# Kernel optimization log

Hardware: AMD Instinct MI355X
Metric: run time of the kernel (lower is better)

Reference implementation:

```python
import jax, jax.numpy as jnp
import numpy as np

B, T, V = 2, 2048, 256
C, H, L = 1024, 16, 8
DH = C // H  # 64


def setup_inputs() -> dict:
    key = jax.random.key(0)
    ks = jax.random.split(key, 12)
    s = 0.02
    return {
        "x": jax.random.normal(ks[0], (B, T, V), jnp.float32),
        "W_emb": jax.random.normal(ks[1], (V, C), jnp.float32) * s,
        "b_emb": jnp.zeros((C,), jnp.float32),
        "pos": jax.random.normal(ks[2], (1, T, C), jnp.float32) * s,
        "Wqkv": jax.random.normal(ks[3], (L, C, 3 * C), jnp.float32) * s,
        "bqkv": jnp.zeros((L, 3 * C), jnp.float32),
        "Wproj": jax.random.normal(ks[4], (L, C, C), jnp.float32) * s,
        "bproj": jnp.zeros((L, C), jnp.float32),
        "gamma": jnp.ones((C,), jnp.float32),
        "beta": jnp.zeros((C,), jnp.float32),
        "W_out": jax.random.normal(ks[5], (C, V), jnp.float32) * s,
        "b_out": jnp.zeros((V,), jnp.float32),
    }


def _attn_block(h, Wqkv_l, bqkv_l, Wproj_l, bproj_l):
    # h: [B, T, C]
    qkv = h @ Wqkv_l + bqkv_l                      # [B, T, 3C]
    q, k, v = jnp.split(qkv, 3, axis=-1)
    q = q.reshape(B, T, H, DH)
    k = k.reshape(B, T, H, DH)
    v = v.reshape(B, T, H, DH)
    scale = 1.0 / np.sqrt(DH).astype(np.float32)
    att = jnp.einsum("bthd,bshd->bhts", q, k) * scale   # [B, H, T, T]
    att = jax.nn.softmax(att, axis=-1)
    y = jnp.einsum("bhts,bshd->bthd", att, v)            # [B, T, H, DH]
    y = y.reshape(B, T, C)
    return y @ Wproj_l + bproj_l


def reference(x, W_emb, b_emb, pos, Wqkv, bqkv, Wproj, bproj, gamma, beta, W_out, b_out):
    h = x @ W_emb + b_emb            # dense embedding: Linear(V -> C)
    h = h + pos[:, :T, :]
    # NOTE: original blocks return attention output directly (no residual, no MLP)
    def body(h, params):
        Wq, bq, Wp, bp = params
        return _attn_block(h, Wq, bq, Wp, bp), None
    h, _ = jax.lax.scan(body, h, (Wqkv, bqkv, Wproj, bproj))
    # LayerNorm
    mu = jnp.mean(h, axis=-1, keepdims=True)
    var = jnp.mean(jnp.square(h - mu), axis=-1, keepdims=True)
    h = (h - mu) * jax.lax.rsqrt(var + 1e-5) * gamma + beta
    return h @ W_out + b_out          # [B, T, V]
```

## Files before the change

### kernel.cpp

```cpp
#include <hip/hip_runtime.h>
#include <hip/hip_bf16.h>

#define T_SEQ 2048
#define BATCH 2
#define CDIM 1024
#define VDIM 256
#define NHEAD 16
#define DHEAD 64
#define NLAYER 8
#define MROWS (BATCH * T_SEQ)

typedef __attribute__((ext_vector_type(8))) short bf16x8;
typedef __attribute__((ext_vector_type(4))) float f32x4;
typedef __attribute__((ext_vector_type(4))) int i32x4;

#define SELHI 0x07060302u
#define SELLO 0x05040100u
#define QSCALE 0.18033688011112042f

__device__ __forceinline__ uint prm(uint a, uint b, uint s) { return __builtin_amdgcn_perm(a, b, s); }

__device__ __forceinline__ uint bf16rne(float f) {
    uint u = __float_as_uint(f);
    return (u + 0x7fffu + ((u >> 16) & 1u)) & 0xffff0000u;
}
__device__ __forceinline__ uint packsplit(float x) {
    uint hb = bf16rne(x);
    float d = x - __uint_as_float(hb);
    uint lb = bf16rne(d);
    return prm(hb, lb, SELHI);
}
__device__ __forceinline__ float unpack2(uint u) {
    return __uint_as_float(u & 0xffff0000u) + __uint_as_float(u << 16);
}
__device__ __forceinline__ bf16x8 asb(i32x4 v) {
    union { i32x4 i; bf16x8 b; } u; u.i = v; return u.b;
}
__device__ __forceinline__ short bfs(float f) { return (short)(bf16rne(f) >> 16); }


__global__ __launch_bounds__(256) void packx_kernel(
    const float* __restrict__ x, uint* __restrict__ xpf)
{
    const int t  = blockIdx.x * 256 + threadIdx.x;
    const int m  = t >> 6;
    const int k0 = (t & 63) * 4;
    const float4 v = *(const float4*)&x[(size_t)m * 256 + k0];
    const size_t addr = ((size_t)(m >> 4) * 8 + (k0 >> 5)) * 512
                      + (size_t)(((k0 >> 2) & 3) * 16 + (m & 15)) * 8
                      + 4 * ((k0 >> 4) & 1);
    uint4 pk;
    pk.x = packsplit(v.x); pk.y = packsplit(v.y);
    pk.z = packsplit(v.z); pk.w = packsplit(v.w);
    *(uint4*)&xpf[addr] = pk;
}

__global__ __launch_bounds__(256) void wsplit_kernel(
    const float* __restrict__ W, short* __restrict__ Fh, short* __restrict__ Fl,
    int N, int K)
{
    const int ln = threadIdx.x & 63, lk = threadIdx.x >> 6;
    const int n  = blockIdx.x * 64 + ln;
    const int kq = blockIdx.y * 4 + lk;
    const int k0 = kq * 4;

    float f0 = W[(size_t)(k0 + 0) * N + n];
    float f1 = W[(size_t)(k0 + 1) * N + n];
    float f2 = W[(size_t)(k0 + 2) * N + n];
    float f3 = W[(size_t)(k0 + 3) * N + n];
    uint h0 = bf16rne(f0), h1 = bf16rne(f1), h2 = bf16rne(f2), h3 = bf16rne(f3);

    const int gl = kq & 3, j0 = ((kq >> 2) & 1) * 4;
    const size_t base = (((size_t)(n >> 4) * (K >> 5) + (kq >> 3)) * 64 + gl * 16 + (n & 15)) * 8 + j0;
    *(int2*)&Fh[base] = make_int2((int)prm(h1, h0, SELHI), (int)prm(h3, h2, SELHI));
    if (Fl) {
        uint l0 = bf16rne(f0 - __uint_as_float(h0));
        uint l1 = bf16rne(f1 - __uint_as_float(h1));
        uint l2 = bf16rne(f2 - __uint_as_float(h2));
        uint l3 = bf16rne(f3 - __uint_as_float(h3));
        *(int2*)&Fl[base] = make_int2((int)prm(l1, l0, SELHI), (int)prm(l3, l2, SELHI));
    }
}

template <int TERMS>
__global__ __launch_bounds__(256) void gemm_mfma_kernel(
    const uint* __restrict__ Apf, const short* __restrict__ Ahf,
    const short* __restrict__ Bhf, const short* __restrict__ Blf,
    const float* __restrict__ bias, const float* __restrict__ addrow,
    uint* __restrict__ Cv, short* __restrict__ Chf,
    uint* __restrict__ Cq, short* __restrict__ Ckf,
    short* __restrict__ Cvf, int M, int N, int K, int out_mode)
{
    const int tid = threadIdx.x, lane = tid & 63, w = tid >> 6;
    const int wr = w >> 1, wc = w & 1, x = lane & 15, gl = lane >> 4;
    const int bm = blockIdx.y * 128, bn = blockIdx.x * 128;
    const int nkc = K >> 5;

    const uint*  ab  = Apf ? Apf + ((size_t)((bm >> 4) + wr * 4) * nkc) * 512 + (size_t)lane * 8 : nullptr;
    const short* abh = Ahf ? Ahf + (((size_t)((bm >> 4) + wr * 4) * nkc) * 64 + lane) * 8 : nullptr;
    const short* hb  = Bhf + (((size_t)((bn >> 4) + wc * 4) * nkc) * 64 + lane) * 8;
    const short* lb  = Blf + (((size_t)((bn >> 4) + wc * 4) * nkc) * 64 + lane) * 8;
    const size_t tstrA = (size_t)nkc * 512;
    const size_t tstrF = (size_t)nkc * 512;

    f32x4 acc[4][4];
#pragma unroll
    for (int mi = 0; mi < 4; ++mi)
#pragma unroll
        for (int ni = 0; ni < 4; ++ni) acc[mi][ni] = (f32x4){0.f, 0.f, 0.f, 0.f};

    for (int kc = 0; kc < nkc; ++kc) {
        const size_t ko = (size_t)kc * 512;
        bf16x8 ah[4], al[4], bh[4], bl[4];
#pragma unroll
        for (int t = 0; t < 4; ++t) {
            if (TERMS == 1) {
                ah[t] = *(const bf16x8*)(abh + t * tstrF + ko);
            } else {
                const uint* ap = ab + t * tstrA + ko;
                uint4 a0 = *(const uint4*)ap;
                uint4 a1 = *(const uint4*)(ap + 4);
                i32x4 h4, l4;
                h4[0] = (int)prm(a0.y, a0.x, SELHI); h4[1] = (int)prm(a0.w, a0.z, SELHI);
                h4[2] = (int)prm(a1.y, a1.x, SELHI); h4[3] = (int)prm(a1.w, a1.z, SELHI);
                l4[0] = (int)prm(a0.y, a0.x, SELLO); l4[1] = (int)prm(a0.w, a0.z, SELLO);
                l4[2] = (int)prm(a1.y, a1.x, SELLO); l4[3] = (int)prm(a1.w, a1.z, SELLO);
                ah[t] = asb(h4); al[t] = asb(l4);
            }
            bh[t] = *(const bf16x8*)(hb + t * tstrF + ko);
            if (TERMS >= 3) bl[t] = *(const bf16x8*)(lb + t * tstrF + ko);
        }
        __builtin_amdgcn_s_setprio(1);
#pragma unroll
        for (int mi = 0; mi < 4; ++mi)
#pragma unroll
            for (int ni = 0; ni < 4; ++ni) {
                acc[mi][ni] = __builtin_amdgcn_mfma_f32_16x16x32_bf16(ah[mi], bh[ni], acc[mi][ni], 0, 0, 0);
                if (TERMS >= 3)
                    acc[mi][ni] = __builtin_amdgcn_mfma_f32_16x16x32_bf16(ah[mi], bl[ni], acc[mi][ni], 0, 0, 0);
                if (TERMS >= 2)
                    acc[mi][ni] = __builtin_amdgcn_mfma_f32_16x16x32_bf16(al[mi], bh[ni], acc[mi][ni], 0, 0, 0);
            }
        __builtin_amdgcn_s_setprio(0);
    }

#pragma unroll
    for (int ni = 0; ni < 4; ++ni) {
        const int n = bn + wc * 64 + ni * 16 + x;
        const float bv = bias[n];
#pragma unroll
        for (int mi = 0; mi < 4; ++mi) {
            const int m0 = bm + wr * 64 + mi * 16 + gl * 4;
            const f32x4 o = acc[mi][ni];
            if (out_mode == 0) {
                float* C = (float*)Cv;
                C[(size_t)(m0 + 0) * N + n] = o[0] + bv;
                C[(size_t)(m0 + 1) * N + n] = o[1] + bv;
                C[(size_t)(m0 + 2) * N + n] = o[2] + bv;
                C[(size_t)(m0 + 3) * N + n] = o[3] + bv;
            } else if (out_mode == 2) {
                float p0 = 0.f, p1 = 0.f, p2 = 0.f, p3 = 0.f;
                if (addrow) {
                    p0 = addrow[(size_t)((m0 + 0) & (T_SEQ - 1)) * N + n];
                    p1 = addrow[(size_t)((m0 + 1) & (T_SEQ - 1)) * N + n];
                    p2 = addrow[(size_t)((m0 + 2) & (T_SEQ - 1)) * N + n];
                    p3 = addrow[(size_t)((m0 + 3) & (T_SEQ - 1)) * N + n];
                }
                const float v0 = o[0] + bv + p0, v1 = o[1] + bv + p1;
                const float v2 = o[2] + bv + p2, v3 = o[3] + bv + p3;
                const size_t mt = (size_t)(bm >> 4) + wr * 4 + mi;
                const size_t base = (mt * (N >> 5) + (n >> 5)) * 512
                                  + (size_t)(((n >> 2) & 3) * 16 + gl * 4) * 8
                                  + (n & 3) + 4 * ((n >> 4) & 1);
                Cv[base + 0 * 8] = packsplit(v0);
                Cv[base + 1 * 8] = packsplit(v1);
                Cv[base + 2 * 8] = packsplit(v2);
                Cv[base + 3 * 8] = packsplit(v3);
                if (Chf) {
                    const size_t fb = ((mt * (N >> 5) + (n >> 5)) * 64
                                      + ((n >> 2) & 3) * 16 + gl * 4) * 8
                                      + (n & 3) + 4 * ((n >> 4) & 1);
                    Chf[fb + 0 * 8] = bfs(v0);
                    Chf[fb + 1 * 8] = bfs(v1);
                    Chf[fb + 2 * 8] = bfs(v2);
                    Chf[fb + 3 * 8] = bfs(v3);
                }
            } else if (n < 1024) {
                Cq[(size_t)(m0 + 0) * 1024 + n] = packsplit((o[0] + bv) * QSCALE);
                Cq[(size_t)(m0 + 1) * 1024 + n] = packsplit((o[1] + bv) * QSCALE);
                Cq[(size_t)(m0 + 2) * 1024 + n] = packsplit((o[2] + bv) * QSCALE);
                Cq[(size_t)(m0 + 3) * 1024 + n] = packsplit((o[3] + bv) * QSCALE);
            } else if (n < 2048) {
                const int dd6 = n - 1024;
                const int hhh = dd6 >> 6, ch = (dd6 >> 5) & 1, dd = dd6 & 31;
                const int bq = m0 >> 11, sv = m0 & (T_SEQ - 1);
                const size_t base = ((((size_t)(bq * NHEAD + hhh) * 128 + (sv >> 4)) * 2 + ch) * 64
                                    + 16 * ((dd & 15) >> 2) + (sv & 15)) * 8
                                    + (dd & 3) + 4 * (dd >> 4);
                Ckf[base + 0]  = bfs(o[0] + bv);
                Ckf[base + 8]  = bfs(o[1] + bv);
                Ckf[base + 16] = bfs(o[2] + bv);
                Ckf[base + 24] = bfs(o[3] + bv);
            } else {
                const int dd6 = n - 2048;
                const int hhh = dd6 >> 6, dmi = (dd6 >> 4) & 3, xt = dd6 & 15;
                const int bq = m0 >> 11, sv = m0 & (T_SEQ - 1);
                const size_t base = ((((size_t)(bq * NHEAD + hhh) * 64 + (sv >> 5)) * 4 + dmi) * 64
                                    + xt + 16 * ((sv & 15) >> 2)) * 8 + 4 * ((sv >> 4) & 1);
                short4 st;
                st.x = bfs(o[0] + bv); st.y = bfs(o[1] + bv);
                st.z = bfs(o[2] + bv); st.w = bfs(o[3] + bv);
                *(short4*)&Cvf[base] = st;
            }
        }
    }
}

__global__ __launch_bounds__(256) void attn_mfma_kernel(
    const uint* __restrict__ qrow, const short* __restrict__ kf,
    const short* __restrict__ vf, uint* __restrict__ y)
{
    const int tid  = threadIdx.x;
    const int w    = tid >> 6;
    const int lane = tid & 63;
    const int x    = lane & 15;
    const int gl   = lane >> 4;

    const int orig = blockIdx.x;
    const int wgid = (orig & 7) * 64 + (orig >> 3);
    const int bh = wgid >> 4;
    const int b = bh >> 4, hh = bh & 15;
    const int t0 = (wgid & 15) * 128;

    i32x4 qhi[2][2];
#pragma unroll
    for (int qf = 0; qf < 2; ++qf) {
        const uint* qp = qrow + (size_t)(b * T_SEQ + t0 + 64 * qf + 16 * w + x) * 1024 + hh * 64;
#pragma unroll
        for (int ch = 0; ch < 2; ++ch) {
            uint4 a0 = *(const uint4*)(qp + 32 * ch + 4 * gl);
            uint4 a1 = *(const uint4*)(qp + 32 * ch + 16 + 4 * gl);
            qhi[qf][ch][0] = (int)prm(a0.y, a0.x, SELHI); qhi[qf][ch][1] = (int)prm(a0.w, a0.z, SELHI);
            qhi[qf][ch][2] = (int)prm(a1.y, a1.x, SELHI); qhi[qf][ch][3] = (int)prm(a1.w, a1.z, SELHI);
        }
    }

    const short* kb = kf + (size_t)bh * 128 * 2 * 512 + (size_t)lane * 8;
    const short* vb = vf + (size_t)bh * 64 * 4 * 512 + (size_t)lane * 8;

    i32x4 ones4;
    ones4[0] = ones4[1] = ones4[2] = ones4[3] = 0x3F803F80;

    f32x4 oacc[2][4], lacc[2];
#pragma unroll
    for (int qf = 0; qf < 2; ++qf) {
        lacc[qf] = (f32x4){0.f, 0.f, 0.f, 0.f};
#pragma unroll
        for (int i = 0; i < 4; ++i) oacc[qf][i] = (f32x4){0.f, 0.f, 0.f, 0.f};
    }

    for (int s0 = 0; s0 < T_SEQ; s0 += 64) {
        bf16x8 kh[4][2], vh[2][4];
#pragma unroll
        for (int sc = 0; sc < 4; ++sc)
#pragma unroll
            for (int ch = 0; ch < 2; ++ch)
                kh[sc][ch] = *(const bf16x8*)(kb + ((((size_t)(s0 >> 4) + sc) * 2 + ch) * 512));
#pragma unroll
        for (int ch = 0; ch < 2; ++ch)
#pragma unroll
            for (int dm = 0; dm < 4; ++dm)
                vh[ch][dm] = *(const bf16x8*)(vb + ((((size_t)(s0 >> 5) + ch) * 4 + dm) * 512));

#pragma unroll
        for (int qf = 0; qf < 2; ++qf) {
            f32x4 s4[4];
#pragma unroll
            for (int sc = 0; sc < 4; ++sc) {
                s4[sc] = (f32x4){0.f, 0.f, 0.f, 0.f};
                s4[sc] = __builtin_amdgcn_mfma_f32_16x16x32_bf16(kh[sc][0], asb(qhi[qf][0]), s4[sc], 0, 0, 0);
                s4[sc] = __builtin_amdgcn_mfma_f32_16x16x32_bf16(kh[sc][1], asb(qhi[qf][1]), s4[sc], 0, 0, 0);
            }
#pragma unroll
            for (int sc = 0; sc < 4; ++sc) {
                s4[sc][0] = __builtin_amdgcn_exp2f(s4[sc][0]);
                s4[sc][1] = __builtin_amdgcn_exp2f(s4[sc][1]);
                s4[sc][2] = __builtin_amdgcn_exp2f(s4[sc][2]);
                s4[sc][3] = __builtin_amdgcn_exp2f(s4[sc][3]);
            }
            i32x4 pfh[2];
#pragma unroll
            for (int c = 0; c < 2; ++c) {
                f32x4 pa = s4[2 * c], pb = s4[2 * c + 1];
                pfh[c][0] = (int)prm(__float_as_uint(pa[1]), __float_as_uint(pa[0]), SELHI);
                pfh[c][1] = (int)prm(__float_as_uint(pa[3]), __float_as_uint(pa[2]), SELHI);
                pfh[c][2] = (int)prm(__float_as_uint(pb[1]), __float_as_uint(pb[0]), SELHI);
                pfh[c][3] = (int)prm(__float_as_uint(pb[3]), __float_as_uint(pb[2]), SELHI);
            }
            lacc[qf] = __builtin_amdgcn_mfma_f32_16x16x32_bf16(asb(ones4), asb(pfh[0]), lacc[qf], 0, 0, 0);
            lacc[qf] = __builtin_amdgcn_mfma_f32_16x16x32_bf16(asb(ones4), asb(pfh[1]), lacc[qf], 0, 0, 0);
#pragma unroll
            for (int dm = 0; dm < 4; ++dm) {
                oacc[qf][dm] = __builtin_amdgcn_mfma_f32_16x16x32_bf16(vh[0][dm], asb(pfh[0]), oacc[qf][dm], 0, 0, 0);
                oacc[qf][dm] = __builtin_amdgcn_mfma_f32_16x16x32_bf16(vh[1][dm], asb(pfh[1]), oacc[qf][dm], 0, 0, 0);
            }
        }
    }

#pragma unroll
    for (int qf = 0; qf < 2; ++qf) {
        const float invl = 1.f / lacc[qf][0];
        const size_t mt = (size_t)((b * T_SEQ + t0) >> 4) + 4 * qf + w;
#pragma unroll
        for (int dm = 0; dm < 4; ++dm) {
            f32x4 o = oacc[qf][dm];
            const size_t addr = (mt * 32 + hh * 2 + (dm >> 1)) * 512
                              + (size_t)lane * 8 + 4 * (dm & 1);
            uint4 pk;
            pk.x = packsplit(o[0] * invl); pk.y = packsplit(o[1] * invl);
            pk.z = packsplit(o[2] * invl); pk.w = packsplit(o[3] * invl);
            *(uint4*)&y[addr] = pk;
        }
    }
}

__global__ __launch_bounds__(256) void ln_kernel(
    const uint* __restrict__ h, const float* __restrict__ gamma,
    const float* __restrict__ beta, uint* __restrict__ outp)
{
    const int row = blockIdx.x;
    const int tid = threadIdx.x;

    const size_t addr = ((size_t)(row >> 4) * 32 + (tid >> 3)) * 512
                      + (size_t)((tid & 3) * 16 + (row & 15)) * 8
                      + 4 * ((tid >> 2) & 1);
    uint4 u = *(const uint4*)&h[addr];
    float4 v;
    v.x = unpack2(u.x); v.y = unpack2(u.y); v.z = unpack2(u.z); v.w = unpack2(u.w);

    float s  = v.x + v.y + v.z + v.w;
    float ss = v.x * v.x + v.y * v.y + v.z * v.z + v.w * v.w;
#pragma unroll
    for (int off = 1; off < 64; off <<= 1) {
        s  += __shfl_xor(s, off);
        ss += __shfl_xor(ss, off);
    }
    __shared__ float rs[4], rss[4];
    const int wid = tid >> 6;
    if ((tid & 63) == 0) { rs[wid] = s; rss[wid] = ss; }
    __syncthreads();
    s  = rs[0] + rs[1] + rs[2] + rs[3];
    ss = rss[0] + rss[1] + rss[2] + rss[3];

    const float mu   = s * (1.f / (float)CDIM);
    const float var  = ss * (1.f / (float)CDIM) - mu * mu;
    const float rstd = rsqrtf(var + 1e-5f);

    const float4 g  = *(const float4*)&gamma[tid * 4];
    const float4 be = *(const float4*)&beta[tid * 4];
    uint4 pk;
    pk.x = packsplit((v.x - mu) * rstd * g.x + be.x);
    pk.y = packsplit((v.y - mu) * rstd * g.y + be.y);
    pk.z = packsplit((v.z - mu) * rstd * g.z + be.z);
    pk.w = packsplit((v.w - mu) * rstd * g.w + be.w);
    *(uint4*)&outp[addr] = pk;
}

extern "C" void kernel_launch(void* const* d_in, const int* in_sizes, int n_in,
                              void* d_out, int out_size, void* d_ws, size_t ws_size,
                              hipStream_t stream)
{
    const float* x      = (const float*)d_in[0];
    const float* W_emb  = (const float*)d_in[1];
    const float* b_emb  = (const float*)d_in[2];
    const float* pos    = (const float*)d_in[3];
    const float* Wqkv   = (const float*)d_in[4];
    const float* bqkv   = (const float*)d_in[5];
    const float* Wproj  = (const float*)d_in[6];
    const float* bproj  = (const float*)d_in[7];
    const float* gamma  = (const float*)d_in[8];
    const float* beta   = (const float*)d_in[9];
    const float* W_out  = (const float*)d_in[10];
    const float* b_out  = (const float*)d_in[11];
    float* out = (float*)d_out;

    uint* h    = (uint*)d_ws;
    uint* qrow = h + (size_t)MROWS * CDIM;
    uint* y    = qrow + (size_t)MROWS * CDIM;
    short* kf  = (short*)(y + (size_t)MROWS * CDIM);
    short* vfb = kf + (size_t)32 * 128 * 2 * 512;
    short* hf  = vfb + (size_t)32 * 64 * 4 * 512;
    short* Bqh = hf + (size_t)MROWS * CDIM;
    short* Bph = Bqh + (size_t)3 * CDIM * CDIM;
    short* Bpl = Bph + (size_t)CDIM * CDIM;
    short* Eh  = Bpl + (size_t)CDIM * CDIM;
    short* El  = Eh  + (size_t)VDIM * CDIM;
    short* Oh  = El  + (size_t)VDIM * CDIM;
    short* Ol  = Oh  + (size_t)CDIM * VDIM;
    uint*  xpf = (uint*)(Ol + (size_t)CDIM * VDIM);

    const dim3 blk(256);
    const int nattn = (T_SEQ / 128) * BATCH * NHEAD;

    packx_kernel<<<dim3(MROWS * (VDIM / 4) / 256), blk, 0, stream>>>(x, xpf);
    wsplit_kernel<<<dim3(CDIM / 64, VDIM / 16), blk, 0, stream>>>(W_emb, Eh, El, CDIM, VDIM);
    gemm_mfma_kernel<3><<<dim3(CDIM / 128, MROWS / 128), blk, 0, stream>>>(
        xpf, nullptr, Eh, El, b_emb, pos, h, hf, nullptr, nullptr, nullptr, MROWS, CDIM, VDIM, 2);

    for (int l = 0; l < NLAYER; ++l) {
        wsplit_kernel<<<dim3(3 * CDIM / 64, CDIM / 16), blk, 0, stream>>>(
            Wqkv + (size_t)l * CDIM * 3 * CDIM, Bqh, nullptr, 3 * CDIM, CDIM);
        gemm_mfma_kernel<1><<<dim3(3 * CDIM / 128, MROWS / 128), blk, 0, stream>>>(
            nullptr, hf, Bqh, nullptr, bqkv + (size_t)l * 3 * CDIM, nullptr,
            nullptr, nullptr, qrow, kf, vfb, MROWS, 3 * CDIM, CDIM, 3);
        attn_mfma_kernel<<<dim3(nattn), blk, 0, stream>>>(qrow, kf, vfb, y);
        wsplit_kernel<<<dim3(CDIM / 64, CDIM / 16), blk, 0, stream>>>(
            Wproj + (size_t)l * CDIM * CDIM, Bph, Bpl, CDIM, CDIM);
        gemm_mfma_kernel<3><<<dim3(CDIM / 128, MROWS / 128), blk, 0, stream>>>(
            y, nullptr, Bph, Bpl, bproj + (size_t)l * CDIM, nullptr,
            h, hf, nullptr, nullptr, nullptr, MROWS, CDIM, CDIM, 2);
    }

    ln_kernel<<<dim3(MROWS), blk, 0, stream>>>(h, gamma, beta, y);
    wsplit_kernel<<<dim3(VDIM / 64, CDIM / 16), blk, 0, stream>>>(W_out, Oh, Ol, VDIM, CDIM);
    gemm_mfma_kernel<3><<<dim3(VDIM / 128, MROWS / 128), blk, 0, stream>>>(
        y, nullptr, Oh, Ol, b_out, nullptr, (uint*)out, nullptr, nullptr, nullptr, nullptr, MROWS, VDIM, CDIM, 0);
}
```

Before: 1.092 ms.

## Stage QKV GEMM operands through LDS via direct global-to-LDS loads

Adds a dedicated single-term QKV projection GEMM in which each k-step copies the A and B fragment tiles into shared memory with global_load_lds, then has the four waves read them from LDS. Previously every wave loaded its own fragments straight from global memory, so each tile was fetched twice per block. Sharing through LDS halves global/L2 traffic per block, at the cost of two barriers per k-step and no double buffering, which may leave load latency exposed. The generic GEMM loses its QKV output mode.

Result: no change. 1.086 ms (-0.6%).

```diff
diff --git a/kernel.cpp b/kernel.cpp
--- a/kernel.cpp
+++ b/kernel.cpp
@@ -37,6 +37,11 @@
     union { i32x4 i; bf16x8 b; } u; u.i = v; return u.b;
 }
 __device__ __forceinline__ short bfs(float f) { return (short)(bf16rne(f) >> 16); }
+__device__ __forceinline__ void gload_lds16(const void* g, void* l) {
+    __builtin_amdgcn_global_load_lds(
+        (const __attribute__((address_space(1))) void*)g,
+        (__attribute__((address_space(3))) void*)l, 16, 0, 0);
+}
 
 
 __global__ __launch_bounds__(256) void packx_kernel(
@@ -82,14 +87,100 @@
     }
 }
 
+__global__ __launch_bounds__(256) void gemm_lds1_kernel(
+    const short* __restrict__ Ahf, const short* __restrict__ Bhf,
+    const float* __restrict__ bias,
+    uint* __restrict__ Cq, short* __restrict__ Ckf, short* __restrict__ Cvf,
+    int M, int N, int K)
+{
+    __shared__ __align__(16) short Asm[8][64][8];
+    __shared__ __align__(16) short Bsm[8][64][8];
+
+    const int tid = threadIdx.x, lane = tid & 63, w = tid >> 6;
+    const int wr = w >> 1, wc = w & 1, x = lane & 15, gl = lane >> 4;
+    const int bm = blockIdx.y * 128, bn = blockIdx.x * 128;
+    const int nkc = K >> 5;
+    const size_t tstr = (size_t)nkc * 512;
+
+    const short* sbase = (w < 2)
+        ? Ahf + ((size_t)((bm >> 4) + 4 * w) * nkc) * 512 + (size_t)lane * 8
+        : Bhf + ((size_t)((bn >> 4) + 4 * (w - 2)) * nkc) * 512 + (size_t)lane * 8;
+    short* dbase = (w < 2) ? &Asm[4 * w][0][0] : &Bsm[4 * (w - 2)][0][0];
+
+    f32x4 acc[4][4];
+#pragma unroll
+    for (int mi = 0; mi < 4; ++mi)
+#pragma unroll
+        for (int ni = 0; ni < 4; ++ni) acc[mi][ni] = (f32x4){0.f, 0.f, 0.f, 0.f};
+
+    for (int kc = 0; kc < nkc; ++kc) {
+        __syncthreads();
+#pragma unroll
+        for (int i = 0; i < 4; ++i)
+            gload_lds16(sbase + i * tstr + (size_t)kc * 512, dbase + i * 512);
+        __syncthreads();
+
+        bf16x8 ah[4], bh[4];
+#pragma unroll
+        for (int t = 0; t < 4; ++t) {
+            ah[t] = *(const bf16x8*)&Asm[wr * 4 + t][lane][0];
+            bh[t] = *(const bf16x8*)&Bsm[wc * 4 + t][lane][0];
+        }
+        __builtin_amdgcn_s_setprio(1);
+#pragma unroll
+        for (int mi = 0; mi < 4; ++mi)
+#pragma unroll
+            for (int ni = 0; ni < 4; ++ni)
+                acc[mi][ni] = __builtin_amdgcn_mfma_f32_16x16x32_bf16(ah[mi], bh[ni], acc[mi][ni], 0, 0, 0);
+        __builtin_amdgcn_s_setprio(0);
+    }
+
+#pragma unroll
+    for (int ni = 0; ni < 4; ++ni) {
+        const int n = bn + wc * 64 + ni * 16 + x;
+        const float bv = bias[n];
+#pragma unroll
+        for (int mi = 0; mi < 4; ++mi) {
+            const int m0 = bm + wr * 64 + mi * 16 + gl * 4;
+            const f32x4 o = acc[mi][ni];
+            if (n < 1024) {
+                Cq[(size_t)(m0 + 0) * 1024 + n] = packsplit((o[0] + bv) * QSCALE);
+                Cq[(size_t)(m0 + 1) * 1024 + n] = packsplit((o[1] + bv) * QSCALE);
+                Cq[(size_t)(m0 + 2) * 1024 + n] = packsplit((o[2] + bv) * QSCALE);
+                Cq[(size_t)(m0 + 3) * 1024 + n] = packsplit((o[3] + bv) * QSCALE);
+            } else if (n < 2048) {
+                const int dd6 = n - 1024;
+                const int hhh = dd6 >> 6, ch = (dd6 >> 5) & 1, dd = dd6 & 31;
+                const int bq = m0 >> 11, sv = m0 & (T_SEQ - 1);
+                const size_t base = ((((size_t)(bq * NHEAD + hhh) * 128 + (sv >> 4)) * 2 + ch) * 64
+                                    + 16 * ((dd & 15) >> 2) + (sv & 15)) * 8
+                                    + (dd & 3) + 4 * (dd >> 4);
+                Ckf[base + 0]  = bfs(o[0] + bv);
+                Ckf[base + 8]  = bfs(o[1] + bv);
+                Ckf[base + 16] = bfs(o[2] + bv);
+                Ckf[base + 24] = bfs(o[3] + bv);
+            } else {
+                const int dd6 = n - 2048;
+                const int hhh = dd6 >> 6, dmi = (dd6 >> 4) & 3, xt = dd6 & 15;
+                const int bq = m0 >> 11, sv = m0 & (T_SEQ - 1);
+                const size_t base = ((((size_t)(bq * NHEAD + hhh) * 64 + (sv >> 5)) * 4 + dmi) * 64
+                                    + xt + 16 * ((sv & 15) >> 2)) * 8 + 4 * ((sv >> 4) & 1);
+                short4 st;
+                st.x = bfs(o[0] + bv); st.y = bfs(o[1] + bv);
+                st.z = bfs(o[2] + bv); st.w = bfs(o[3] + bv);
+                *(short4*)&Cvf[base] = st;
+            }
+        }
+    }
+}
+
 template <int TERMS>
 __global__ __launch_bounds__(256) void gemm_mfma_kernel(
     const uint* __restrict__ Apf, const short* __restrict__ Ahf,
     const short* __restrict__ Bhf, const short* __restrict__ Blf,
     const float* __restrict__ bias, const float* __restrict__ addrow,
     uint* __restrict__ Cv, short* __restrict__ Chf,
-    uint* __restrict__ Cq, short* __restrict__ Ckf,
-    short* __restrict__ Cvf, int M, int N, int K, int out_mode)
+    int M, int N, int K, int out_mode)
 {
     const int tid = threadIdx.x, lane = tid & 63, w = tid >> 6;
     const int wr = w >> 1, wc = w & 1, x = lane & 15, gl = lane >> 4;
@@ -158,7 +249,7 @@
                 C[(size_t)(m0 + 1) * N + n] = o[1] + bv;
                 C[(size_t)(m0 + 2) * N + n] = o[2] + bv;
                 C[(size_t)(m0 + 3) * N + n] = o[3] + bv;
-            } else if (out_mode == 2) {
+            } else {
                 float p0 = 0.f, p1 = 0.f, p2 = 0.f, p3 = 0.f;
                 if (addrow) {
                     p0 = addrow[(size_t)((m0 + 0) & (T_SEQ - 1)) * N + n];
@@ -185,32 +276,6 @@
                     Chf[fb + 2 * 8] = bfs(v2);
                     Chf[fb + 3 * 8] = bfs(v3);
                 }
-            } else if (n < 1024) {
-                Cq[(size_t)(m0 + 0) * 1024 + n] = packsplit((o[0] + bv) * QSCALE);
-                Cq[(size_t)(m0 + 1) * 1024 + n] = packsplit((o[1] + bv) * QSCALE);
-                Cq[(size_t)(m0 + 2) * 1024 + n] = packsplit((o[2] + bv) * QSCALE);
-                Cq[(size_t)(m0 + 3) * 1024 + n] = packsplit((o[3] + bv) * QSCALE);
-            } else if (n < 2048) {
-                const int dd6 = n - 1024;
-                const int hhh = dd6 >> 6, ch = (dd6 >> 5) & 1, dd = dd6 & 31;
-                const int bq = m0 >> 11, sv = m0 & (T_SEQ - 1);
-                const size_t base = ((((size_t)(bq * NHEAD + hhh) * 128 + (sv >> 4)) * 2 + ch) * 64
-                                    + 16 * ((dd & 15) >> 2) + (sv & 15)) * 8
-                                    + (dd & 3) + 4 * (dd >> 4);
-                Ckf[base + 0]  = bfs(o[0] + bv);
-                Ckf[base + 8]  = bfs(o[1] + bv);
-                Ckf[base + 16] = bfs(o[2] + bv);
-                Ckf[base + 24] = bfs(o[3] + bv);
-            } else {
-                const int dd6 = n - 2048;
-                const int hhh = dd6 >> 6, dmi = (dd6 >> 4) & 3, xt = dd6 & 15;
-                const int bq = m0 >> 11, sv = m0 & (T_SEQ - 1);
-                const size_t base = ((((size_t)(bq * NHEAD + hhh) * 64 + (sv >> 5)) * 4 + dmi) * 64
-                                    + xt + 16 * ((sv & 15) >> 2)) * 8 + 4 * ((sv >> 4) & 1);
-                short4 st;
-                st.x = bfs(o[0] + bv); st.y = bfs(o[1] + bv);
-                st.z = bfs(o[2] + bv); st.w = bfs(o[3] + bv);
-                *(short4*)&Cvf[base] = st;
             }
         }
     }
@@ -405,24 +470,23 @@
     packx_kernel<<<dim3(MROWS * (VDIM / 4) / 256), blk, 0, stream>>>(x, xpf);
     wsplit_kernel<<<dim3(CDIM / 64, VDIM / 16), blk, 0, stream>>>(W_emb, Eh, El, CDIM, VDIM);
     gemm_mfma_kernel<3><<<dim3(CDIM / 128, MROWS / 128), blk, 0, stream>>>(
-        xpf, nullptr, Eh, El, b_emb, pos, h, hf, nullptr, nullptr, nullptr, MROWS, CDIM, VDIM, 2);
+        xpf, nullptr, Eh, El, b_emb, pos, h, hf, MROWS, CDIM, VDIM, 2);
 
     for (int l = 0; l < NLAYER; ++l) {
         wsplit_kernel<<<dim3(3 * CDIM / 64, CDIM / 16), blk, 0, stream>>>(
             Wqkv + (size_t)l * CDIM * 3 * CDIM, Bqh, nullptr, 3 * CDIM, CDIM);
-        gemm_mfma_kernel<1><<<dim3(3 * CDIM / 128, MROWS / 128), blk, 0, stream>>>(
-            nullptr, hf, Bqh, nullptr, bqkv + (size_t)l * 3 * CDIM, nullptr,
-            nullptr, nullptr, qrow, kf, vfb, MROWS, 3 * CDIM, CDIM, 3);
+        gemm_lds1_kernel<<<dim3(3 * CDIM / 128, MROWS / 128), blk, 0, stream>>>(
+            hf, Bqh, bqkv + (size_t)l * 3 * CDIM, qrow, kf, vfb, MROWS, 3 * CDIM, CDIM);
         attn_mfma_kernel<<<dim3(nattn), blk, 0, stream>>>(qrow, kf, vfb, y);
         wsplit_kernel<<<dim3(CDIM / 64, CDIM / 16), blk, 0, stream>>>(
             Wproj + (size_t)l * CDIM * CDIM, Bph, Bpl, CDIM, CDIM);
         gemm_mfma_kernel<3><<<dim3(CDIM / 128, MROWS / 128), blk, 0, stream>>>(
             y, nullptr, Bph, Bpl, bproj + (size_t)l * CDIM, nullptr,
-            h, hf, nullptr, nullptr, nullptr, MROWS, CDIM, CDIM, 2);
+            h, hf, MROWS, CDIM, CDIM, 2);
     }
 
     ln_kernel<<<dim3(MROWS), blk, 0, stream>>>(h, gamma, beta, y);
     wsplit_kernel<<<dim3(VDIM / 64, CDIM / 16), blk, 0, stream>>>(W_out, Oh, Ol, VDIM, CDIM);
     gemm_mfma_kernel<3><<<dim3(VDIM / 128, MROWS / 128), blk, 0, stream>>>(
-        y, nullptr, Oh, Ol, b_out, nullptr, (uint*)out, nullptr, nullptr, nullptr, nullptr, MROWS, VDIM, CDIM, 0);
-}
+        y, nullptr, Oh, Ol, b_out, nullptr, (uint*)out, nullptr, MROWS, VDIM, CDIM, 0);
+}
```
